# Kernel tuning notes

Hardware: AMD Instinct MI355X
Metric: run time of the kernel (lower is better)

Reference implementation:

```python
import jax, jax.numpy as jnp
import numpy as np
import itertools
from jax import lax

B, CIN, COUT, RES, NH = 32, 512, 512, 56, 8
STRIDE = RES // 7  # 8 -> post-stride grid is 7x7 (N=49)
HD = COUT // NH    # 64


def _affine(x, s, b):  # BatchNorm2d in inference form (per-channel scale/shift)
    return x * s[None, :, None, None] + b[None, :, None, None]


def _conv1x1(x, w):  # w: [O, C]
    return jnp.einsum('oc,bchw->bohw', w, x)


def _conv3x3(x, w, stride, groups):
    return lax.conv_general_dilated(
        x, w, window_strides=(stride, stride), padding=[(1, 1), (1, 1)],
        feature_group_count=groups, dimension_numbers=('NCHW', 'OIHW', 'NCHW'))


def _bias_idx():
    points = list(itertools.product(range(7), range(7)))
    offsets, idxs = {}, []
    for p1 in points:
        for p2 in points:
            off = (abs(p1[0] - p2[0]), abs(p1[1] - p2[1]))
            if off not in offsets:
                offsets[off] = len(offsets)
            idxs.append(offsets[off])
    return np.array(idxs, dtype=np.int32).reshape(49, 49), len(offsets)


def setup_inputs() -> dict:
    key = jax.random.key(0)
    ks = jax.random.split(key, 24)
    idx_np, n_off = _bias_idx()  # n_off = 49
    rn = lambda k, sh, sc: jax.random.normal(k, sh, dtype=jnp.float32) * sc
    return {
        'x': rn(ks[0], (B, CIN, RES, RES), 1.0),
        'dw_w': rn(ks[1], (CIN, 1, 3, 3), 0.2),
        'bn0_s': 1.0 + rn(ks[2], (CIN,), 0.05), 'bn0_b': rn(ks[3], (CIN,), 0.05),
        'wq': rn(ks[4], (COUT, CIN), 0.03),
        'bnq_s': 1.0 + rn(ks[5], (COUT,), 0.05), 'bnq_b': rn(ks[6], (COUT,), 0.05),
        'wk': rn(ks[7], (COUT, CIN), 0.03),
        'bnk_s': 1.0 + rn(ks[8], (COUT,), 0.05), 'bnk_b': rn(ks[9], (COUT,), 0.05),
        'wv': rn(ks[10], (COUT, CIN), 0.03),
        'bnv_s': 1.0 + rn(ks[11], (COUT,), 0.05), 'bnv_b': rn(ks[12], (COUT,), 0.05),
        'loc_w': rn(ks[13], (COUT, COUT // NH, 3, 3), 0.05), 'loc_b': rn(ks[14], (COUT,), 0.02),
        'bnl_s': 1.0 + rn(ks[15], (COUT,), 0.05), 'bnl_b': rn(ks[16], (COUT,), 0.05),
        'th1': rn(ks[17], (NH, NH), 0.3), 'th2': rn(ks[18], (NH, NH), 0.3),
        'logit_scale': jnp.log(10.0) * jnp.ones((NH, 1, 1), dtype=jnp.float32),
        'ab': rn(ks[19], (NH, n_off), 0.02),
        'wo': rn(ks[20], (COUT, COUT), 0.03),
        'bno_s': 1.0 + rn(ks[21], (COUT,), 0.05), 'bno_b': rn(ks[22], (COUT,), 0.05),
        'bias_idx': jnp.array(idx_np),
    }


def reference(x, dw_w, bn0_s, bn0_b, wq, bnq_s, bnq_b, wk, bnk_s, bnk_b,
              wv, bnv_s, bnv_b, loc_w, loc_b, bnl_s, bnl_b, th1, th2,
              logit_scale, ab, wo, bno_s, bno_b, bias_idx):
    # stride_conv: depthwise 3x3 stride-8 + BN -> [B, C, 7, 7]
    x = _affine(_conv3x3(x, dw_w, STRIDE, CIN), bn0_s, bn0_b)
    Bc, C, H, W = x.shape
    N = H * W  # 49
    q = _affine(_conv1x1(x, wq), bnq_s, bnq_b).reshape(Bc, NH, HD, N).transpose(0, 1, 3, 2)  # [B,H,N,d]
    k = _affine(_conv1x1(x, wk), bnk_s, bnk_b).reshape(Bc, NH, HD, N)                        # [B,H,d,N]
    v4 = _affine(_conv1x1(x, wv), bnv_s, bnv_b)                                              # [B,Cout,7,7]
    v_local = _affine(_conv3x3(v4, loc_w, 1, NH) + loc_b[None, :, None, None], bnl_s, bnl_b)
    v = v4.reshape(Bc, NH, HD, N).transpose(0, 1, 3, 2)                                      # [B,H,N,d]
    # faithful to source: q normalized over head_dim, k normalized over token axis (last)
    qn = q / jnp.maximum(jnp.linalg.norm(q, axis=-1, keepdims=True), 1e-12)
    kn = k / jnp.maximum(jnp.linalg.norm(k, axis=-1, keepdims=True), 1e-12)
    ls = jnp.exp(jnp.minimum(logit_scale, jnp.log(100.0)))  # clamp max then exp
    attn = jnp.einsum('bhnd,bhdm->bhnm', qn, kn) * ls + ab[:, bias_idx]  # [B,H,49,49]
    attn = jnp.einsum('ij,bjnm->binm', th1, attn)   # talking head 1
    attn = jax.nn.softmax(attn, axis=-1)
    attn = jnp.einsum('ij,bjnm->binm', th2, attn)   # talking head 2
    out = jnp.einsum('bhnm,bhmd->bhnd', attn, v)    # [B,H,N,d]
    out = out.transpose(0, 1, 3, 2).reshape(Bc, COUT, H, W) + v_local
    out = jax.image.resize(out, (Bc, COUT, H * STRIDE, W * STRIDE), method='bilinear')
    out = out * jax.nn.relu6(out + 3.0) / 6.0       # Hardswish
    return _affine(_conv1x1(out, wo), bno_s, bno_b)
```

## Files before the change

kernel.cpp:

```cpp
#include <hip/hip_runtime.h>
#include <hip/hip_bf16.h>
#include <stdint.h>

typedef short short8 __attribute__((ext_vector_type(8)));
typedef float f32x4 __attribute__((ext_vector_type(4)));

#define NB    32
#define NC    512
#define NHD   8
#define HDD   64
#define N7    49
#define RES   56
#define P56   3136
#define NTOK  1568
#define NTOKP 1664
#define NBIG  100352
#define KDIM  512
#define KLOC  576

__device__ __forceinline__ void gload_lds16(const __hip_bfloat16* g, __hip_bfloat16* l) {
  __builtin_amdgcn_global_load_lds(
      (const __attribute__((address_space(1))) void*)g,
      (__attribute__((address_space(3))) void*)l, 16, 0, 0);
}

__global__ __launch_bounds__(256) void k_stride_cvt(
    const float* __restrict__ x, const float* __restrict__ dw,
    const float* __restrict__ s0, const float* __restrict__ b0,
    __hip_bfloat16* __restrict__ xs,
    const float* __restrict__ c0, const float* __restrict__ c1,
    const float* __restrict__ c2, const float* __restrict__ c3,
    const float* __restrict__ c4,
    __hip_bfloat16* __restrict__ d0, __hip_bfloat16* __restrict__ d1,
    __hip_bfloat16* __restrict__ d2, __hip_bfloat16* __restrict__ d3,
    __hip_bfloat16* __restrict__ d4) {
  const int bid = blockIdx.x, t = threadIdx.x;
  if (bid >= 4096) {
    const long base = (long)(bid - 4096) * 2048;
#pragma unroll
    for (int j = 0; j < 8; ++j) {
      long i = base + t + j * 256;
      const float* s; __hip_bfloat16* d; long off;
      if (i >= 1048576)      { s = c4; d = d4; off = i - 1048576; }
      else if (i >= 786432)  { s = c3; d = d3; off = i - 786432; }
      else if (i >= 524288)  { s = c2; d = d2; off = i - 524288; }
      else if (i >= 262144)  { s = c1; d = d1; off = i - 262144; }
      else                   { s = c0; d = d0; off = i; }
      d[off] = __float2bfloat16(s[off]);
    }
    return;
  }
  const int b = bid >> 7, cig = bid & 127;
  const int sub = t >> 6, lane = t & 63;
  const int ci = cig * 4 + sub;
  __shared__ float rows[4][21][56];
  const float* xp = x + ((size_t)(b * NC + ci)) * RES * RES;
  for (int r = lane; r < 21 * 56; r += 64) {
    int rr = r / 56, cc = r - rr * 56;
    int oh = rr / 3, kh = rr - oh * 3;
    int ih = oh * 8 + kh - 1;
    rows[sub][rr][cc] = (ih >= 0) ? xp[ih * 56 + cc] : 0.f;
  }
  float w[9];
#pragma unroll
  for (int j = 0; j < 9; ++j) w[j] = dw[ci * 9 + j];
  const float sc = s0[ci], bi = b0[ci];
  __syncthreads();
  if (lane < 49) {
    const int oh = lane / 7, ow = lane - oh * 7;
    float acc = 0.f;
#pragma unroll
    for (int kh = 0; kh < 3; ++kh)
#pragma unroll
      for (int kw = 0; kw < 3; ++kw) {
        int col = ow * 8 + kw - 1;
        float v = (col >= 0) ? rows[sub][oh * 3 + kh][col] : 0.f;
        acc += v * w[kh * 3 + kw];
      }
    xs[(size_t)(b * 49 + lane) * NC + ci] = __float2bfloat16(acc * sc + bi);
  }
}

__global__ __launch_bounds__(512) void k_gemm_big(
    const __hip_bfloat16* __restrict__ A,
    const __hip_bfloat16* __restrict__ Bm,
    const float* __restrict__ scale, const float* __restrict__ bias,
    float* __restrict__ out) {
  __shared__ __align__(16) __hip_bfloat16 lsA[2][256 * 32];
  __shared__ __align__(16) __hip_bfloat16 lsB[2][256 * 32];
  const int t = threadIdx.x;
  const int cpx = gridDim.x >> 3;
  const int nid = (blockIdx.x & 7) * cpx + (blockIdx.x >> 3);
  const int m0 = (nid & 1) * 256, n0 = (nid >> 1) * 256;

  const int lane = t & 63, wid = t >> 6;
  const int wm = (wid >> 2) * 128, wn = (wid & 3) * 64;
  const int fr = lane & 15, fq = lane >> 4;
  const int rslot = (fq ^ ((fr >> 1) & 3)) * 8;

  const int srow = t >> 2;
  const int scol = ((t & 3) ^ ((t >> 3) & 3)) * 8;
  const __hip_bfloat16* Ab = A  + (size_t)(m0 + srow) * KDIM + scol;
  const __hip_bfloat16* Bb = Bm + (size_t)(n0 + srow) * KDIM + scol;

  const f32x4 fz = {0.f, 0.f, 0.f, 0.f};
  f32x4 acc[8][4];
#pragma unroll
  for (int i = 0; i < 8; ++i)
#pragma unroll
    for (int j = 0; j < 4; ++j) acc[i][j] = fz;

#define STA(tile, call) gload_lds16(Ab + (tile) * 32 + (size_t)(call) * 128 * KDIM, \
                                    lsA[(tile) & 1] + (call) * 4096 + wid * 512)
#define STB(tile, call) gload_lds16(Bb + (tile) * 32 + (size_t)(call) * 128 * KDIM, \
                                    lsB[(tile) & 1] + (call) * 4096 + wid * 512)

  STA(0, 0); STA(0, 1); STB(0, 0); STB(0, 1);
  STA(1, 0); STA(1, 1); STB(1, 0); STB(1, 1);

#pragma unroll 1
  for (int tt = 0; tt < 16; ++tt) {
    if (tt < 15) asm volatile("s_waitcnt vmcnt(4)" ::: "memory");
    else         asm volatile("s_waitcnt vmcnt(0)" ::: "memory");
    __builtin_amdgcn_sched_barrier(0);
    __builtin_amdgcn_s_barrier();
    __builtin_amdgcn_sched_barrier(0);

    const __hip_bfloat16* lA = lsA[tt & 1];
    const __hip_bfloat16* lB = lsB[tt & 1];
    short8 af[4], ag[4], bf[4];
#pragma unroll
    for (int i = 0; i < 4; ++i)
      af[i] = *(const short8*)(lA + (wm + i * 16 + fr) * 32 + rslot);
#pragma unroll
    for (int i = 0; i < 4; ++i)
      ag[i] = *(const short8*)(lA + (wm + 64 + i * 16 + fr) * 32 + rslot);
#pragma unroll
    for (int j = 0; j < 4; ++j)
      bf[j] = *(const short8*)(lB + (wn + j * 16 + fr) * 32 + rslot);
    __builtin_amdgcn_s_setprio(1);
#pragma unroll
    for (int i = 0; i < 4; ++i)
#pragma unroll
      for (int j = 0; j < 4; ++j)
        acc[i][j] = __builtin_amdgcn_mfma_f32_16x16x32_bf16(af[i], bf[j], acc[i][j], 0, 0, 0);
#pragma unroll
    for (int i = 0; i < 4; ++i)
#pragma unroll
      for (int j = 0; j < 4; ++j)
        acc[4 + i][j] = __builtin_amdgcn_mfma_f32_16x16x32_bf16(ag[i], bf[j], acc[4 + i][j], 0, 0, 0);
    __builtin_amdgcn_s_setprio(0);

    __builtin_amdgcn_sched_barrier(0);
    __builtin_amdgcn_s_barrier();
    __builtin_amdgcn_sched_barrier(0);
    if (tt < 14) { STA(tt + 2, 0); STA(tt + 2, 1); STB(tt + 2, 0); STB(tt + 2, 1); }
  }
#undef STA
#undef STB

#pragma unroll
  for (int mi = 0; mi < 8; ++mi) {
#pragma unroll
    for (int ni = 0; ni < 4; ++ni) {
      const int gn = n0 + wn + ni * 16 + fr;
      const int outer = gn / P56;
      const int ii = gn - outer * P56;
#pragma unroll
      for (int r = 0; r < 4; ++r) {
        const int co = m0 + wm + mi * 16 + fq * 4 + r;
        out[((size_t)outer * NC + co) * P56 + ii] = acc[mi][ni][r] * scale[co] + bias[co];
      }
    }
  }
}

__global__ __launch_bounds__(256) void k_gemm_qkv(
    const __hip_bfloat16* __restrict__ wqb, const __hip_bfloat16* __restrict__ wkb,
    const __hip_bfloat16* __restrict__ wvb, const __hip_bfloat16* __restrict__ xs,
    const float* __restrict__ sq, const float* __restrict__ bq,
    const float* __restrict__ sk, const float* __restrict__ bk,
    const float* __restrict__ sv, const float* __restrict__ bv,
    float* __restrict__ qb, float* __restrict__ kb, float* __restrict__ vb) {
  __shared__ __align__(16) __hip_bfloat16 lsA[2][128 * 32];
  __shared__ __align__(16) __hip_bfloat16 lsB[2][128 * 32];
  const int t = threadIdx.x;
  const int nwg = gridDim.x;
  const int orig = blockIdx.x;
  const int q = nwg >> 3, r = nwg & 7;
  const int xcd = orig & 7, pos = orig >> 3;
  const int nid = (xcd < r ? xcd * (q + 1) : r * (q + 1) + (xcd - r) * q) + pos;
  const int mt = nid % 12, nt = nid / 12;
  const int n0 = nt * 128, m0 = (mt & 3) * 128, sel = mt >> 2;

  const __hip_bfloat16* A = (sel == 0 ? wqb : sel == 1 ? wkb : wvb);
  const float* scale = (sel == 0 ? sq : sel == 1 ? sk : sv);
  const float* bias  = (sel == 0 ? bq : sel == 1 ? bk : bv);
  float* out = (sel == 0 ? qb : sel == 1 ? kb : vb);

  const int lane = t & 63, wid = t >> 6;
  const int wm = (wid >> 1) * 64, wn = (wid & 1) * 64;
  const int fr = lane & 15, fq = lane >> 4;
  const int rslot = (fq ^ ((fr >> 1) & 3)) * 8;
  const int srow = t >> 2;
  const int scol = ((t & 3) ^ ((t >> 3) & 3)) * 8;
  const __hip_bfloat16* Ab = A  + (size_t)(m0 + srow) * KDIM + scol;
  const __hip_bfloat16* Bb = xs + (size_t)(n0 + srow) * KDIM + scol;

  const f32x4 fz = {0.f, 0.f, 0.f, 0.f};
  f32x4 acc[4][4];
#pragma unroll
  for (int i = 0; i < 4; ++i)
#pragma unroll
    for (int j = 0; j < 4; ++j) acc[i][j] = fz;

#define STG_QKV(tile)                                                   \
  do {                                                                  \
    const int kof = (tile) * 32; const int bb = (tile) & 1;             \
    gload_lds16(Ab + kof,                       lsA[bb] + wid * 512);   \
    gload_lds16(Ab + kof + (size_t)64 * KDIM,   lsA[bb] + 2048 + wid * 512); \
    gload_lds16(Bb + kof,                       lsB[bb] + wid * 512);   \
    gload_lds16(Bb + kof + (size_t)64 * KDIM,   lsB[bb] + 2048 + wid * 512); \
  } while (0)

  STG_QKV(0);
  STG_QKV(1);
#pragma unroll 1
  for (int it = 0; it < 16; ++it) {
    if (it < 15) asm volatile("s_waitcnt vmcnt(4)" ::: "memory");
    else         asm volatile("s_waitcnt vmcnt(0)" ::: "memory");
    __builtin_amdgcn_sched_barrier(0);
    __builtin_amdgcn_s_barrier();
    __builtin_amdgcn_sched_barrier(0);
    const __hip_bfloat16* lA = lsA[it & 1];
    const __hip_bfloat16* lB = lsB[it & 1];
    short8 af[4], bf[4];
#pragma unroll
    for (int mi = 0; mi < 4; ++mi)
      af[mi] = *(const short8*)(lA + (wm + mi * 16 + fr) * 32 + rslot);
#pragma unroll
    for (int ni = 0; ni < 4; ++ni)
      bf[ni] = *(const short8*)(lB + (wn + ni * 16 + fr) * 32 + rslot);
#pragma unroll
    for (int mi = 0; mi < 4; ++mi)
#pragma unroll
      for (int ni = 0; ni < 4; ++ni)
        acc[mi][ni] = __builtin_amdgcn_mfma_f32_16x16x32_bf16(af[mi], bf[ni], acc[mi][ni], 0, 0, 0);
    __builtin_amdgcn_sched_barrier(0);
    __builtin_amdgcn_s_barrier();
    __builtin_amdgcn_sched_barrier(0);
    if (it < 14) STG_QKV(it + 2);
  }
#undef STG_QKV

#pragma unroll
  for (int mi = 0; mi < 4; ++mi) {
#pragma unroll
    for (int ni = 0; ni < 4; ++ni) {
      const int gn = n0 + wn + ni * 16 + fr;
      if (gn >= NTOK) continue;
      const int b = gn / 49, ii = gn - b * 49;
#pragma unroll
      for (int r = 0; r < 4; ++r) {
        const int co = m0 + wm + mi * 16 + fq * 4 + r;
        out[((size_t)b * NC + co) * 49 + ii] = acc[mi][ni][r] * scale[co] + bias[co];
      }
    }
  }
}

__global__ __launch_bounds__(256) void k_im2col(
    const float* __restrict__ vb, __hip_bfloat16* __restrict__ bloc) {
  const int g = blockIdx.x, b = blockIdx.y, t = threadIdx.x;
  __shared__ __hip_bfloat16 pad[64][81];
  for (int i = t; i < 64 * 81; i += 256) pad[i / 81][i % 81] = __float2bfloat16(0.f);
  __syncthreads();
  const float* src = vb + ((size_t)b * NC + g * 64) * 49;
  for (int i = t; i < 64 * 49; i += 256) {
    const int ci = i / 49, n = i - ci * 49;
    const int oh = n / 7, ow = n - oh * 7;
    pad[ci][(oh + 1) * 9 + (ow + 1)] = __float2bfloat16(src[i]);
  }
  __syncthreads();
  __hip_bfloat16* dst = bloc + ((size_t)g * NTOKP + (size_t)b * 49) * KLOC;
  for (int i = t; i < 49 * KLOC; i += 256) {
    const int n = i / KLOC, k = i - n * KLOC;
    const int ci = k / 9, tap = k - ci * 9;
    const int kh = tap / 3, kw = tap - kh * 3;
    const int oh = n / 7, ow = n - oh * 7;
    dst[i] = pad[ci][(oh + kh) * 9 + (ow + kw)];
  }
}

__global__ __launch_bounds__(256) void k_vloc_gemm(
    const __hip_bfloat16* __restrict__ lwb,
    const __hip_bfloat16* __restrict__ bloc,
    const float* __restrict__ lbias, const float* __restrict__ sl,
    const float* __restrict__ bl, float* __restrict__ vloc) {
  __shared__ __align__(16) __hip_bfloat16 lsA[2][64 * 32];
  __shared__ __align__(16) __hip_bfloat16 lsB[2][128 * 32];
  const int t = threadIdx.x;
  const int g = blockIdx.y;
  const int n0 = blockIdx.x * 128;
  const int lane = t & 63, wid = t >> 6;
  const int wm = (wid >> 1) * 32, wn = (wid & 1) * 64;
  const int fr = lane & 15, fq = lane >> 4;
  const int rslot = (fq ^ ((fr >> 1) & 3)) * 8;
  const int srow = t >> 2;
  const int scol = ((t & 3) ^ ((t >> 3) & 3)) * 8;
  const __hip_bfloat16* Ab = lwb  + ((size_t)g * 64 + srow) * KLOC + scol;
  const __hip_bfloat16* Bb = bloc + ((size_t)g * NTOKP + n0 + srow) * KLOC + scol;

  const f32x4 fz = {0.f, 0.f, 0.f, 0.f};
  f32x4 acc[2][4];
#pragma unroll
  for (int i = 0; i < 2; ++i)
#pragma unroll
    for (int j = 0; j < 4; ++j) acc[i][j] = fz;

#define STG_VL(tile)                                                     \
  do {                                                                   \
    const int kof = (tile) * 32; const int bb = (tile) & 1;              \
    gload_lds16(Ab + kof,                      lsA[bb] + wid * 512);     \
    gload_lds16(Bb + kof,                      lsB[bb] + wid * 512);     \
    gload_lds16(Bb + kof + (size_t)64 * KLOC,  lsB[bb] + 2048 + wid * 512); \
  } while (0)

  STG_VL(0);
  STG_VL(1);
#pragma unroll 1
  for (int it = 0; it < 18; ++it) {
    if (it < 17) asm volatile("s_waitcnt vmcnt(3)" ::: "memory");
    else         asm volatile("s_waitcnt vmcnt(0)" ::: "memory");
    __builtin_amdgcn_sched_barrier(0);
    __builtin_amdgcn_s_barrier();
    __builtin_amdgcn_sched_barrier(0);
    const __hip_bfloat16* lA = lsA[it & 1];
    const __hip_bfloat16* lB = lsB[it & 1];
    short8 af[2], bf[4];
#pragma unroll
    for (int mi = 0; mi < 2; ++mi)
      af[mi] = *(const short8*)(lA + (wm + mi * 16 + fr) * 32 + rslot);
#pragma unroll
    for (int ni = 0; ni < 4; ++ni)
      bf[ni] = *(const short8*)(lB + (wn + ni * 16 + fr) * 32 + rslot);
#pragma unroll
    for (int mi = 0; mi < 2; ++mi)
#pragma unroll
      for (int ni = 0; ni < 4; ++ni)
        acc[mi][ni] = __builtin_amdgcn_mfma_f32_16x16x32_bf16(af[mi], bf[ni], acc[mi][ni], 0, 0, 0);
    __builtin_amdgcn_sched_barrier(0);
    __builtin_amdgcn_s_barrier();
    __builtin_amdgcn_sched_barrier(0);
    if (it < 16) STG_VL(it + 2);
  }
#undef STG_VL

#pragma unroll
  for (int mi = 0; mi < 2; ++mi) {
#pragma unroll
    for (int ni = 0; ni < 4; ++ni) {
      const int gn = n0 + wn + ni * 16 + fr;
      if (gn >= NTOK) continue;
      const int b = gn / 49, n = gn - b * 49;
#pragma unroll
      for (int r = 0; r < 4; ++r) {
        const int oc = g * 64 + wm + mi * 16 + fq * 4 + r;
        const float sc = sl[oc];
        vloc[((size_t)b * NC + oc) * 49 + n] = acc[mi][ni][r] * sc + lbias[oc] * sc + bl[oc];
      }
    }
  }
}

__global__ __launch_bounds__(256) void k_attn1(
    const float* __restrict__ qb, const float* __restrict__ kb,
    const float* __restrict__ lsc, const float* __restrict__ ab, const int* __restrict__ bidx,
    float* __restrict__ Sbuf) {
  const int h = blockIdx.x, b = blockIdx.y, t = threadIdx.x;
  __shared__ float qt[64 * 49], kt[64 * 49], nq[49], abl[49];
  const float* qs = qb + ((size_t)b * NC + h * 64) * 49;
  const float* ks = kb + ((size_t)b * NC + h * 64) * 49;
  for (int i = t; i < 64 * 49; i += 256) { qt[i] = qs[i]; kt[i] = ks[i]; }
  if (t < 49) abl[t] = ab[h * 49 + t];
  __syncthreads();
  if (t < 49) {
    float s = 0.f;
    for (int d = 0; d < 64; ++d) { float v = qt[d * 49 + t]; s += v * v; }
    nq[t] = fmaxf(sqrtf(s), 1e-12f);
  } else if (t >= 64 && t < 128) {
    const int d = t - 64;
    float s = 0.f;
    for (int m = 0; m < 49; ++m) { float v = kt[d * 49 + m]; s += v * v; }
    const float inv = 1.f / fmaxf(sqrtf(s), 1e-12f);
    for (int m = 0; m < 49; ++m) kt[d * 49 + m] *= inv;
  }
  __syncthreads();
  const float ls = expf(fminf(lsc[h], logf(100.f)));
  for (int idx = t; idx < 49 * 49; idx += 256) {
    const int n = idx / 49, m = idx - n * 49;
    float acc = 0.f;
    for (int d = 0; d < 64; ++d) acc += qt[d * 49 + n] * kt[d * 49 + m];
    Sbuf[(((size_t)b * NHD + h) * 49 + n) * 49 + m] = acc / nq[n] * ls + abl[bidx[idx]];
  }
}

__global__ __launch_bounds__(256) void k_attn2(
    const float* __restrict__ Sbuf, const float* __restrict__ th1, const float* __restrict__ th2,
    const float* __restrict__ vb, const float* __restrict__ vloc, float* __restrict__ y7) {
  const int n = blockIdx.x, b = blockIdx.y, t = threadIdx.x;
  __shared__ float sS[8][49], sP[8][49], sQ[8][49];
  __shared__ float t1[64], t2[64], rsuminv[8];
  if (t < 64) { t1[t] = th1[t]; t2[t] = th2[t]; }
  for (int i = t; i < 392; i += 256) {
    const int j = i / 49, m = i - j * 49;
    sS[j][m] = Sbuf[(((size_t)b * NHD + j) * 49 + n) * 49 + m];
  }
  __syncthreads();
  for (int i = t; i < 392; i += 256) {
    const int j = i / 49, m = i - j * 49;
    float a = 0.f;
#pragma unroll
    for (int jj = 0; jj < 8; ++jj) a += t1[j * 8 + jj] * sS[jj][m];
    sP[j][m] = a;
  }
  __syncthreads();
  if (t < 8) {
    float mx = -1e30f;
    for (int m = 0; m < 49; ++m) mx = fmaxf(mx, sP[t][m]);
    float s = 0.f;
    for (int m = 0; m < 49; ++m) { float e = expf(sP[t][m] - mx); sP[t][m] = e; s += e; }
    rsuminv[t] = 1.f / s;
  }
  __syncthreads();
  for (int i = t; i < 392; i += 256) {
    const int j = i / 49, m = i - j * 49;
    float a = 0.f;
#pragma unroll
    for (int jj = 0; jj < 8; ++jj) a += t2[j * 8 + jj] * (sP[jj][m] * rsuminv[jj]);
    sQ[j][m] = a;
  }
  __syncthreads();
  for (int c = t; c < NC; c += 256) {
    const int hh = c >> 6;
    const float* vp = vb + ((size_t)b * NC + c) * 49;
    float a = 0.f;
    for (int m = 0; m < 49; ++m) a += sQ[hh][m] * vp[m];
    a += vloc[((size_t)b * NC + c) * 49 + n];
    y7[((size_t)b * 49 + n) * NC + c] = a;
  }
}

__global__ __launch_bounds__(256) void k_resize(const float* __restrict__ y7,
                                                __hip_bfloat16* __restrict__ h) {
  const int y = blockIdx.x, b = blockIdx.y, t = threadIdx.x;
  __shared__ float L[2][7][512];
  float sy = (y - 3.5f) * 0.125f;
  sy = fminf(fmaxf(sy, 0.f), 6.f);
  const int iy0 = min((int)floorf(sy), 5);
  const float wy = sy - (float)iy0;
  const float* src = y7 + ((size_t)b * 49 + iy0 * 7) * NC;
  float* Lf = &L[0][0][0];
  for (int i = t; i < 2 * 7 * 512; i += 256) Lf[i] = src[i];
  __syncthreads();
  const size_t outb = ((size_t)b * P56 + (size_t)y * 56) * NC;
  const int cg = (t & 63) * 8;
  const int xq = t >> 6;
  for (int x0 = 0; x0 < 56; x0 += 4) {
    const int x = x0 + xq;
    float sx = (x - 3.5f) * 0.125f;
    sx = fminf(fmaxf(sx, 0.f), 6.f);
    const int ix0 = min((int)floorf(sx), 5);
    const float wx = sx - (float)ix0;
    const float w00 = (1.f - wy) * (1.f - wx), w01 = (1.f - wy) * wx;
    const float w10 = wy * (1.f - wx),         w11 = wy * wx;
    short8 pk;
#pragma unroll
    for (int j = 0; j < 8; ++j) {
      const int c = cg + j;
      const float v = w00 * L[0][ix0][c] + w01 * L[0][ix0 + 1][c]
                    + w10 * L[1][ix0][c] + w11 * L[1][ix0 + 1][c];
      const float hs = v * fminf(fmaxf(v + 3.f, 0.f), 6.f) * (1.f / 6.f);
      pk[j] = (short)__bfloat16_as_ushort(__float2bfloat16(hs));
    }
    *(short8*)(&h[outb + (size_t)x * NC + cg]) = pk;
  }
}

extern "C" void kernel_launch(void* const* d_in, const int* in_sizes, int n_in,
                              void* d_out, int out_size, void* d_ws, size_t ws_size,
                              hipStream_t stream) {
  (void)in_sizes; (void)n_in; (void)out_size; (void)ws_size;
  const float* x     = (const float*)d_in[0];
  const float* dw_w  = (const float*)d_in[1];
  const float* bn0_s = (const float*)d_in[2];
  const float* bn0_b = (const float*)d_in[3];
  const float* wq    = (const float*)d_in[4];
  const float* bnq_s = (const float*)d_in[5];
  const float* bnq_b = (const float*)d_in[6];
  const float* wk    = (const float*)d_in[7];
  const float* bnk_s = (const float*)d_in[8];
  const float* bnk_b = (const float*)d_in[9];
  const float* wv    = (const float*)d_in[10];
  const float* bnv_s = (const float*)d_in[11];
  const float* bnv_b = (const float*)d_in[12];
  const float* loc_w = (const float*)d_in[13];
  const float* loc_b = (const float*)d_in[14];
  const float* bnl_s = (const float*)d_in[15];
  const float* bnl_b = (const float*)d_in[16];
  const float* th1   = (const float*)d_in[17];
  const float* th2   = (const float*)d_in[18];
  const float* lsc   = (const float*)d_in[19];
  const float* ab    = (const float*)d_in[20];
  const float* wo    = (const float*)d_in[21];
  const float* bno_s = (const float*)d_in[22];
  const float* bno_b = (const float*)d_in[23];
  const int*   bidx  = (const int*)d_in[24];

  char* w = (char*)d_ws;
  auto alloc = [&](size_t bytes) {
    char* p = w;
    w += (bytes + 255) & ~(size_t)255;
    return p;
  };
  __hip_bfloat16* h_buf = (__hip_bfloat16*)alloc((size_t)NBIG * NC * 2);
  __hip_bfloat16* wq_b  = (__hip_bfloat16*)alloc((size_t)NC * NC * 2);
  __hip_bfloat16* wk_b  = (__hip_bfloat16*)alloc((size_t)NC * NC * 2);
  __hip_bfloat16* wv_b  = (__hip_bfloat16*)alloc((size_t)NC * NC * 2);
  __hip_bfloat16* wo_b  = (__hip_bfloat16*)alloc((size_t)NC * NC * 2);
  __hip_bfloat16* lw_b  = (__hip_bfloat16*)alloc((size_t)NC * KLOC * 2);
  __hip_bfloat16* xs    = (__hip_bfloat16*)alloc((size_t)NTOKP * NC * 2);
  float* qb   = (float*)alloc((size_t)NB * NC * 49 * 4);
  float* kb   = (float*)alloc((size_t)NB * NC * 49 * 4);
  float* vb   = (float*)alloc((size_t)NB * NC * 49 * 4);
  float* vloc = (float*)alloc((size_t)NB * NC * 49 * 4);
  float* y7   = (float*)alloc((size_t)NB * 49 * NC * 4);
  float* Sb   = (float*)alloc((size_t)NB * NHD * 49 * 49 * 4);
  __hip_bfloat16* bloc = (__hip_bfloat16*)h_buf;

  k_stride_cvt<<<dim3(4096 + 656), 256, 0, stream>>>(
      x, dw_w, bn0_s, bn0_b, xs,
      wq, wk, wv, wo, loc_w, wq_b, wk_b, wv_b, wo_b, lw_b);
  k_gemm_qkv<<<dim3(13 * 12), 256, 0, stream>>>(wq_b, wk_b, wv_b, xs,
                                                bnq_s, bnq_b, bnk_s, bnk_b, bnv_s, bnv_b,
                                                qb, kb, vb);
  k_im2col<<<dim3(NHD, NB), 256, 0, stream>>>(vb, bloc);
  k_vloc_gemm<<<dim3(13, NHD), 256, 0, stream>>>(lw_b, bloc, loc_b, bnl_s, bnl_b, vloc);
  k_attn1<<<dim3(NHD, NB), 256, 0, stream>>>(qb, kb, lsc, ab, bidx, Sb);
  k_attn2<<<dim3(49, NB), 256, 0, stream>>>(Sb, th1, th2, vb, vloc, y7);
  k_resize<<<dim3(RES, NB), 256, 0, stream>>>(y7, h_buf);
  k_gemm_big<<<dim3(784), 512, 0, stream>>>(wo_b, h_buf, bno_s, bno_b, (float*)d_out);
}
```

Baseline: 262.5 us.

## Fuse bilinear resize and hardswish into output GEMM B-tile staging

Removes the separate resize kernel and its roughly 100 MB bf16 intermediate. The final 1x1-conv GEMM now builds its B tiles on the fly: it bilinearly interpolates from the small y7 buffer, applies hardswish, and writes bf16 into LDS. Per-token offsets and weights are precomputed into shared memory. This saves a large write and read of HBM traffic, but puts synchronous global loads and ALU work inside the GEMM's staging path, which can stall the MFMA pipeline. The y7 reads are redundant across blocks.

```diff
diff --git a/kernel.cpp b/kernel.cpp
--- a/kernel.cpp
+++ b/kernel.cpp
@@ -83,11 +83,13 @@
 
 __global__ __launch_bounds__(512) void k_gemm_big(
     const __hip_bfloat16* __restrict__ A,
-    const __hip_bfloat16* __restrict__ Bm,
+    const float* __restrict__ y7,
     const float* __restrict__ scale, const float* __restrict__ bias,
     float* __restrict__ out) {
   __shared__ __align__(16) __hip_bfloat16 lsA[2][256 * 32];
   __shared__ __align__(16) __hip_bfloat16 lsB[2][256 * 32];
+  __shared__ int   toff[256][4];
+  __shared__ float twt[256][4];
   const int t = threadIdx.x;
   const int cpx = gridDim.x >> 3;
   const int nid = (blockIdx.x & 7) * cpx + (blockIdx.x >> 3);
@@ -100,8 +102,63 @@
 
   const int srow = t >> 2;
   const int scol = ((t & 3) ^ ((t >> 3) & 3)) * 8;
-  const __hip_bfloat16* Ab = A  + (size_t)(m0 + srow) * KDIM + scol;
-  const __hip_bfloat16* Bb = Bm + (size_t)(n0 + srow) * KDIM + scol;
+  const __hip_bfloat16* Ab = A + (size_t)(m0 + srow) * KDIM + scol;
+
+  if (t < 256) {
+    const int gn = n0 + t;
+    const int q6 = gn >> 6;
+    const int b = (q6 * 1338) >> 16;
+    const int p = gn - b * P56;
+    const int y = (p * 9363) >> 19;
+    const int xx = p - y * 56;
+    float sy = fminf(fmaxf((y - 3.5f) * 0.125f, 0.f), 6.f);
+    float sx = fminf(fmaxf((xx - 3.5f) * 0.125f, 0.f), 6.f);
+    const int iy0 = min((int)sy, 5), ix0 = min((int)sx, 5);
+    const float wy = sy - (float)iy0, wx = sx - (float)ix0;
+    const int base = (b * N7 + iy0 * 7 + ix0) * NC;
+    toff[t][0] = base;             twt[t][0] = (1.f - wy) * (1.f - wx);
+    toff[t][1] = base + NC;        twt[t][1] = (1.f - wy) * wx;
+    toff[t][2] = base + 7 * NC;    twt[t][2] = wy * (1.f - wx);
+    toff[t][3] = base + 8 * NC;    twt[t][3] = wy * wx;
+  }
+  __syncthreads();
+
+  const int brow = t >> 1, cg = (t & 1) * 16;
+  const int bsw = ((brow >> 1) & 3);
+  const int o0 = toff[brow][0], o1 = toff[brow][1], o2 = toff[brow][2], o3 = toff[brow][3];
+  const float w0 = twt[brow][0], w1 = twt[brow][1], w2 = twt[brow][2], w3 = twt[brow][3];
+
+#define STAGE_B(tile)                                                        \
+  do {                                                                       \
+    const int kb = (tile) * 32 + cg;                                         \
+    const float* p0 = y7 + o0 + kb;                                          \
+    const float* p1 = y7 + o1 + kb;                                          \
+    const float* p2 = y7 + o2 + kb;                                          \
+    const float* p3 = y7 + o3 + kb;                                          \
+    short8 pk0, pk1;                                                         \
+    _Pragma("unroll")                                                        \
+    for (int j = 0; j < 8; ++j) {                                            \
+      float v = w0 * p0[j] + w1 * p1[j] + w2 * p2[j] + w3 * p3[j];           \
+      v = v * fminf(fmaxf(v + 3.f, 0.f), 6.f) * (1.f / 6.f);                 \
+      pk0[j] = (short)__bfloat16_as_ushort(__float2bfloat16(v));             \
+    }                                                                        \
+    _Pragma("unroll")                                                        \
+    for (int j = 0; j < 8; ++j) {                                            \
+      float v = w0 * p0[8 + j] + w1 * p1[8 + j] + w2 * p2[8 + j] + w3 * p3[8 + j]; \
+      v = v * fminf(fmaxf(v + 3.f, 0.f), 6.f) * (1.f / 6.f);                 \
+      pk1[j] = (short)__bfloat16_as_ushort(__float2bfloat16(v));             \
+    }                                                                        \
+    __hip_bfloat16* dst = lsB[(tile) & 1] + brow * 32;                       \
+    const int c16 = cg >> 3;                                                 \
+    *(short8*)(dst + ((c16) ^ bsw) * 8) = pk0;                               \
+    *(short8*)(dst + ((c16 + 1) ^ bsw) * 8) = pk1;                           \
+  } while (0)
+
+#define STAGE_A(tile)                                                              \
+  do {                                                                             \
+    gload_lds16(Ab + (tile) * 32,                       lsA[(tile) & 1] + wid * 512); \
+    gload_lds16(Ab + (tile) * 32 + (size_t)128 * KDIM,  lsA[(tile) & 1] + 4096 + wid * 512); \
+  } while (0)
 
   const f32x4 fz = {0.f, 0.f, 0.f, 0.f};
   f32x4 acc[8][4];
@@ -110,18 +167,16 @@
 #pragma unroll
     for (int j = 0; j < 4; ++j) acc[i][j] = fz;
 
-#define STA(tile, call) gload_lds16(Ab + (tile) * 32 + (size_t)(call) * 128 * KDIM, \
-                                    lsA[(tile) & 1] + (call) * 4096 + wid * 512)
-#define STB(tile, call) gload_lds16(Bb + (tile) * 32 + (size_t)(call) * 128 * KDIM, \
-                                    lsB[(tile) & 1] + (call) * 4096 + wid * 512)
-
-  STA(0, 0); STA(0, 1); STB(0, 0); STB(0, 1);
-  STA(1, 0); STA(1, 1); STB(1, 0); STB(1, 1);
+  STAGE_B(0);
+  STAGE_B(1);
+  STAGE_A(0);
+  asm volatile("s_waitcnt vmcnt(0)" ::: "memory");
+  STAGE_A(1);
 
 #pragma unroll 1
   for (int tt = 0; tt < 16; ++tt) {
-    if (tt < 15) asm volatile("s_waitcnt vmcnt(4)" ::: "memory");
-    else         asm volatile("s_waitcnt vmcnt(0)" ::: "memory");
+    if (tt == 15) asm volatile("s_waitcnt vmcnt(0)" ::: "memory");
+    asm volatile("s_waitcnt lgkmcnt(0)" ::: "memory");
     __builtin_amdgcn_sched_barrier(0);
     __builtin_amdgcn_s_barrier();
     __builtin_amdgcn_sched_barrier(0);
@@ -154,10 +209,13 @@
     __builtin_amdgcn_sched_barrier(0);
     __builtin_amdgcn_s_barrier();
     __builtin_amdgcn_sched_barrier(0);
-    if (tt < 14) { STA(tt + 2, 0); STA(tt + 2, 1); STB(tt + 2, 0); STB(tt + 2, 1); }
-  }
-#undef STA
-#undef STB
+    if (tt < 14) {
+      STAGE_B(tt + 2);
+      STAGE_A(tt + 2);
+    }
+  }
+#undef STAGE_A
+#undef STAGE_B
 
 #pragma unroll
   for (int mi = 0; mi < 8; ++mi) {
@@ -448,42 +506,6 @@
     for (int m = 0; m < 49; ++m) a += sQ[hh][m] * vp[m];
     a += vloc[((size_t)b * NC + c) * 49 + n];
     y7[((size_t)b * 49 + n) * NC + c] = a;
-  }
-}
-
-__global__ __launch_bounds__(256) void k_resize(const float* __restrict__ y7,
-                                                __hip_bfloat16* __restrict__ h) {
-  const int y = blockIdx.x, b = blockIdx.y, t = threadIdx.x;
-  __shared__ float L[2][7][512];
-  float sy = (y - 3.5f) * 0.125f;
-  sy = fminf(fmaxf(sy, 0.f), 6.f);
-  const int iy0 = min((int)floorf(sy), 5);
-  const float wy = sy - (float)iy0;
-  const float* src = y7 + ((size_t)b * 49 + iy0 * 7) * NC;
-  float* Lf = &L[0][0][0];
-  for (int i = t; i < 2 * 7 * 512; i += 256) Lf[i] = src[i];
-  __syncthreads();
-  const size_t outb = ((size_t)b * P56 + (size_t)y * 56) * NC;
-  const int cg = (t & 63) * 8;
-  const int xq = t >> 6;
-  for (int x0 = 0; x0 < 56; x0 += 4) {
-    const int x = x0 + xq;
-    float sx = (x - 3.5f) * 0.125f;
-    sx = fminf(fmaxf(sx, 0.f), 6.f);
-    const int ix0 = min((int)floorf(sx), 5);
-    const float wx = sx - (float)ix0;
-    const float w00 = (1.f - wy) * (1.f - wx), w01 = (1.f - wy) * wx;
-    const float w10 = wy * (1.f - wx),         w11 = wy * wx;
-    short8 pk;
-#pragma unroll
-    for (int j = 0; j < 8; ++j) {
-      const int c = cg + j;
-      const float v = w00 * L[0][ix0][c] + w01 * L[0][ix0 + 1][c]
-                    + w10 * L[1][ix0][c] + w11 * L[1][ix0 + 1][c];
-      const float hs = v * fminf(fmaxf(v + 3.f, 0.f), 6.f) * (1.f / 6.f);
-      pk[j] = (short)__bfloat16_as_ushort(__float2bfloat16(hs));
-    }
-    *(short8*)(&h[outb + (size_t)x * NC + cg]) = pk;
   }
 }
 
@@ -523,20 +545,19 @@
     w += (bytes + 255) & ~(size_t)255;
     return p;
   };
-  __hip_bfloat16* h_buf = (__hip_bfloat16*)alloc((size_t)NBIG * NC * 2);
   __hip_bfloat16* wq_b  = (__hip_bfloat16*)alloc((size_t)NC * NC * 2);
   __hip_bfloat16* wk_b  = (__hip_bfloat16*)alloc((size_t)NC * NC * 2);
   __hip_bfloat16* wv_b  = (__hip_bfloat16*)alloc((size_t)NC * NC * 2);
   __hip_bfloat16* wo_b  = (__hip_bfloat16*)alloc((size_t)NC * NC * 2);
   __hip_bfloat16* lw_b  = (__hip_bfloat16*)alloc((size_t)NC * KLOC * 2);
   __hip_bfloat16* xs    = (__hip_bfloat16*)alloc((size_t)NTOKP * NC * 2);
+  __hip_bfloat16* bloc  = (__hip_bfloat16*)alloc((size_t)NHD * NTOKP * KLOC * 2);
   float* qb   = (float*)alloc((size_t)NB * NC * 49 * 4);
   float* kb   = (float*)alloc((size_t)NB * NC * 49 * 4);
   float* vb   = (float*)alloc((size_t)NB * NC * 49 * 4);
   float* vloc = (float*)alloc((size_t)NB * NC * 49 * 4);
   float* y7   = (float*)alloc((size_t)NB * 49 * NC * 4);
   float* Sb   = (float*)alloc((size_t)NB * NHD * 49 * 49 * 4);
-  __hip_bfloat16* bloc = (__hip_bfloat16*)h_buf;
 
   k_stride_cvt<<<dim3(4096 + 656), 256, 0, stream>>>(
       x, dw_w, bn0_s, bn0_b, xs,
@@ -548,6 +569,5 @@
   k_vloc_gemm<<<dim3(13, NHD), 256, 0, stream>>>(lw_b, bloc, loc_b, bnl_s, bnl_b, vloc);
   k_attn1<<<dim3(NHD, NB), 256, 0, stream>>>(qb, kb, lsc, ab, bidx, Sb);
   k_attn2<<<dim3(49, NB), 256, 0, stream>>>(Sb, th1, th2, vb, vloc, y7);
-  k_resize<<<dim3(RES, NB), 256, 0, stream>>>(y7, h_buf);
-  k_gemm_big<<<dim3(784), 512, 0, stream>>>(wo_b, h_buf, bno_s, bno_b, (float*)d_out);
-}
+  k_gemm_big<<<dim3(784), 512, 0, stream>>>(wo_b, y7, bno_s, bno_b, (float*)d_out);
+}
```

After: 303.2 us. 15.5% more time.
